# Kernel tuning notes

Hardware: AMD Instinct MI355X
Metric: run time of the kernel (lower is better)

The kernel has to match this reference:

```python
import jax, jax.numpy as jnp
import numpy as np

NUM_HEADS = 12
AGENT_NUM = 49

def setup_inputs() -> dict:
    key = jax.random.key(0)
    ks = jax.random.split(key, 5)
    B, N, C = 32, 1176, 768
    x = jax.random.normal(ks[0], (B, N, C), dtype=jnp.float32)
    qkv_w = jax.random.normal(ks[1], (3 * C, C), dtype=jnp.float32) * 0.02
    qkv_b = jax.random.normal(ks[2], (3 * C,), dtype=jnp.float32) * 0.02
    proj_w = jax.random.normal(ks[3], (C, C), dtype=jnp.float32) * 0.02
    proj_b = jax.random.normal(ks[4], (C,), dtype=jnp.float32) * 0.02
    return {"x": x, "qkv_w": qkv_w, "qkv_b": qkv_b, "proj_w": proj_w,
            "proj_b": proj_b, "t_h": 14, "t_w": 14, "s_h": 28, "s_w": 28}

def _softmax_clamped(a):
    # original: float32 clamp to finfo min/max, then softmax(dim=-1)
    fi = jnp.finfo(jnp.float32)
    a = jnp.clip(a.astype(jnp.float32), fi.min, fi.max)
    return jax.nn.softmax(a, axis=-1)

def reference(x, qkv_w, qkv_b, proj_w, proj_b, t_h, t_w, s_h, s_w):
    B, N, C = x.shape
    H = NUM_HEADS
    hd = C // H
    scale = hd ** -0.5
    n_mt = 2 * t_h * t_w
    n_s = s_h * s_w

    qkv = (x @ qkv_w.T + qkv_b).reshape(B, N, 3, H, hd).transpose(2, 0, 3, 1, 4)
    q, k, v = qkv[0], qkv[1], qkv[2]  # [B,H,N,hd]

    q_mt, q_s = q[:, :, :n_mt], q[:, :, n_mt:]
    k_mt = k[:, :, :n_mt]
    v_mt = v[:, :, :n_mt]

    # stage 1: template/memory self-attention
    attn = _softmax_clamped(jnp.einsum('bhqd,bhkd->bhqk', q_mt, k_mt) * scale)
    x_mt = jnp.einsum('bhqk,bhkd->bhqd', attn, v_mt).transpose(0, 2, 1, 3).reshape(B, n_mt, C)

    # agent tokens: pool q_s (replicates original layout-scrambling reshape)
    p = int(AGENT_NUM ** 0.5)  # 7
    agent = q_s.reshape(B, s_h, s_w, C).transpose(0, 3, 1, 2)  # [B,C,s_h,s_w]
    agent = agent.reshape(B, C, p, s_h // p, p, s_w // p).mean(axis=(3, 5))  # exact AdaptiveAvgPool2d(7,7)
    agent = agent.reshape(B, C, AGENT_NUM).transpose(0, 2, 1)  # [B,agent_num,C]
    agent = agent.reshape(B, AGENT_NUM, H, hd).transpose(0, 2, 1, 3)  # [B,H,agent_num,hd]

    # stage 2: agent attends to all keys
    agent_attn = _softmax_clamped(jnp.einsum('bhad,bhkd->bhak', agent * scale, k))
    agent_v = jnp.einsum('bhak,bhkd->bhad', agent_attn, v)  # [B,H,agent_num,hd]

    # stage 3: search queries attend to agent tokens
    q_attn = _softmax_clamped(jnp.einsum('bhqd,bhad->bhqa', q_s * scale, agent))
    x_s = jnp.einsum('bhqa,bhad->bhqd', q_attn, agent_v).transpose(0, 2, 1, 3).reshape(B, n_s, C)

    out = jnp.concatenate([x_mt, x_s], axis=1)
    out = out @ proj_w.T + proj_b
    return out
```

## Files before the change

### kernel.cpp

```cpp
#include <hip/hip_runtime.h>

typedef __attribute__((ext_vector_type(8))) short short8;
typedef __attribute__((ext_vector_type(4))) short short4v;
typedef __attribute__((ext_vector_type(4))) float f32x4;
typedef unsigned short u16;

#define B_    32
#define N_    1176
#define C_    768
#define H_    12
#define HD_   64
#define NMT_  392
#define AG_   49
#define NEGBIG_ (-1.0e4f)

__device__ __forceinline__ u16 f2bf(float f) {
  unsigned u = __float_as_uint(f);
  unsigned r = (u + 0x7fffu + ((u >> 16) & 1u)) >> 16;
  return (u16)r;
}
__device__ __forceinline__ float bf2f(u16 s) {
  return __uint_as_float(((unsigned)s) << 16);
}

__device__ __forceinline__ int xcd_swz(int g, int nwg) {
  const int q = nwg >> 3, r = nwg & 7;
  const int xcd = g & 7, off = g >> 3;
  return (xcd < r ? xcd * (q + 1) : r * (q + 1) + (xcd - r) * q) + off;
}

template <int LO>
__global__ __launch_bounds__(256) void splitf(const float* __restrict__ in,
                                              u16* __restrict__ hi,
                                              u16* __restrict__ lo, int n4) {
  int i = blockIdx.x * 256 + threadIdx.x;
  const int stride = gridDim.x * 256;
  for (; i < n4; i += stride) {
    const float4 v = ((const float4*)in)[i];
    const float f[4] = {v.x, v.y, v.z, v.w};
    short4v h, l;
#pragma unroll
    for (int e = 0; e < 4; ++e) {
      u16 hb = f2bf(f[e]);
      h[e] = (short)hb;
      if (LO) l[e] = (short)f2bf(f[e] - bf2f(hb));
    }
    ((short4v*)hi)[i] = h;
    if (LO) ((short4v*)lo)[i] = l;
  }
}

__global__ __launch_bounds__(256, 3) void gemm_qkv(
    const u16* __restrict__ A, const u16* __restrict__ Bw,
    const float* __restrict__ bias, u16* __restrict__ qb, u16* __restrict__ kb,
    u16* __restrict__ vb, int Mch) {
  __shared__ u16 SH[17408];
  u16* As = SH;
  u16* Bs = SH + 4096;
  const int tid = threadIdx.x;
  const int swz = xcd_swz(blockIdx.x, gridDim.x);
  const int brow = swz / 18, bcol = swz - brow * 18;
  const int m0 = brow * 128, c0 = bcol * 128;
  const int lane = tid & 63, w = tid >> 6;
  const int wr = w >> 1, wc = w & 1;
  const int fr = lane & 15, ko = lane >> 4;

  f32x4 acc[4][4];
#pragma unroll
  for (int m = 0; m < 4; ++m)
#pragma unroll
    for (int n = 0; n < 4; ++n) acc[m][n] = (f32x4)0.f;

  short8 ra[2], rb[2];
  auto LOADG = [&](int kt) {
#pragma unroll
    for (int i = 0; i < 2; ++i) {
      const int ch = tid + i * 256;
      const int row = ch >> 2, slot = ch & 3;
      const int ar = min(m0 + row, Mch - 1);
      ra[i] = *(const short8*)&A[(size_t)ar * 768 + kt * 32 + slot * 8];
      rb[i] = *(const short8*)&Bw[(size_t)(c0 + row) * 768 + kt * 32 + slot * 8];
    }
  };
  auto WRITE = [&]() {
#pragma unroll
    for (int i = 0; i < 2; ++i) {
      const int ch = tid + i * 256;
      const int row = ch >> 2, slot = ch & 3;
      const int off = (row >> 4) * 512 + slot * 128 + (row & 15) * 8;
      *(short8*)&As[off] = ra[i];
      *(short8*)&Bs[off] = rb[i];
    }
  };

  LOADG(0);
  for (int kt = 0; kt < 24; ++kt) {
    __syncthreads();
    WRITE();
    if (kt < 23) LOADG(kt + 1);
    __syncthreads();
    short8 af[4], bfr[4];
#pragma unroll
    for (int m = 0; m < 4; ++m) af[m] = *(const short8*)&As[(wr * 4 + m) * 512 + lane * 8];
#pragma unroll
    for (int n = 0; n < 4; ++n) bfr[n] = *(const short8*)&Bs[(wc * 4 + n) * 512 + lane * 8];
#pragma unroll
    for (int m = 0; m < 4; ++m)
#pragma unroll
      for (int n = 0; n < 4; ++n)
        acc[m][n] = __builtin_amdgcn_mfma_f32_16x16x32_bf16(af[m], bfr[n], acc[m][n], 0, 0, 0);
  }

  __syncthreads();
  const int t = c0 / 768;
  const int hbase = (c0 % 768) >> 6;
  if (t < 2) {
#pragma unroll
    for (int n = 0; n < 4; ++n) {
      const int col = wc * 64 + n * 16 + fr;
      const float bv = bias[c0 + col];
#pragma unroll
      for (int m = 0; m < 4; ++m)
#pragma unroll
        for (int r = 0; r < 4; ++r) {
          const int row = wr * 64 + m * 16 + ko * 4 + r;
          SH[row * 136 + col] = f2bf(acc[m][n][r] + bv);
        }
    }
    __syncthreads();
    u16* dst = (t == 0) ? qb : kb;
    for (int it = tid; it < 2048; it += 256) {
      const int rt = it >> 4, half = (it >> 3) & 1, p = it & 7;
      const int mg = m0 + rt;
      if (mg < Mch) {
        const int bl = mg / N_, nt = mg - bl * N_;
        const short8 vv = *(const short8*)&SH[rt * 136 + half * 64 + p * 8];
        *(short8*)&dst[(((size_t)bl * H_ + hbase + half) * N_ + nt) * 64 + p * 8] = vv;
      }
    }
  } else {
#pragma unroll
    for (int n = 0; n < 4; ++n) {
      const int col = wc * 64 + n * 16 + fr;
      const float bv = bias[c0 + col];
#pragma unroll
      for (int m = 0; m < 4; ++m)
#pragma unroll
        for (int r = 0; r < 4; ++r) {
          const int row = wr * 64 + m * 16 + ko * 4 + r;
          SH[col * 136 + row] = f2bf(acc[m][n][r] + bv);
        }
    }
    __syncthreads();
    for (int it = tid; it < 2048; it += 256) {
      const int ct = it >> 4, tc = it & 15;
      const int mg0 = m0 + tc * 8;
      if (mg0 < Mch) {
        const int bl = mg0 / N_, nt = mg0 - bl * N_;
        const int d = ct & 63, hh = hbase + (ct >> 6);
        const short8 vv = *(const short8*)&SH[ct * 136 + tc * 8];
        *(short8*)&vb[(((size_t)bl * H_ + hh) * 64 + d) * N_ + nt] = vv;
      }
    }
  }
}

__global__ __launch_bounds__(256, 2) void gemm_proj(
    const u16* __restrict__ Ahg, const u16* __restrict__ Alg,
    const u16* __restrict__ Bhg, const u16* __restrict__ Blg,
    const float* __restrict__ bias, float* __restrict__ out) {
  __shared__ u16 Ah[4096], Al[4096], Bh[4096], Bl[4096];
  const int tid = threadIdx.x;
  const int swz = xcd_swz(blockIdx.x, gridDim.x);
  const int brow = swz / 6, bcol = swz - brow * 6;
  const int m0 = brow * 128, c0 = bcol * 128;
  const int lane = tid & 63, w = tid >> 6;
  const int wr = w >> 1, wc = w & 1;
  const int fr = lane & 15, ko = lane >> 4;

  f32x4 acc[4][4];
#pragma unroll
  for (int m = 0; m < 4; ++m)
#pragma unroll
    for (int n = 0; n < 4; ++n) acc[m][n] = (f32x4)0.f;

  short8 rah[2], ral[2], rbh[2], rbl[2];
  auto LOADG = [&](int kt) {
#pragma unroll
    for (int i = 0; i < 2; ++i) {
      const int ch = tid + i * 256;
      const int row = ch >> 2, slot = ch & 3;
      const size_t aoff = (size_t)(m0 + row) * 768 + kt * 32 + slot * 8;
      const size_t boff = (size_t)(c0 + row) * 768 + kt * 32 + slot * 8;
      rah[i] = *(const short8*)&Ahg[aoff];
      ral[i] = *(const short8*)&Alg[aoff];
      rbh[i] = *(const short8*)&Bhg[boff];
      rbl[i] = *(const short8*)&Blg[boff];
    }
  };
  auto WRITE = [&]() {
#pragma unroll
    for (int i = 0; i < 2; ++i) {
      const int ch = tid + i * 256;
      const int row = ch >> 2, slot = ch & 3;
      const int off = (row >> 4) * 512 + slot * 128 + (row & 15) * 8;
      *(short8*)&Ah[off] = rah[i];
      *(short8*)&Al[off] = ral[i];
      *(short8*)&Bh[off] = rbh[i];
      *(short8*)&Bl[off] = rbl[i];
    }
  };

  LOADG(0);
  for (int kt = 0; kt < 24; ++kt) {
    __syncthreads();
    WRITE();
    if (kt < 23) LOADG(kt + 1);
    __syncthreads();
    short8 ah[4], al[4], bh[4], bl[4];
#pragma unroll
    for (int m = 0; m < 4; ++m) {
      ah[m] = *(const short8*)&Ah[(wr * 4 + m) * 512 + lane * 8];
      al[m] = *(const short8*)&Al[(wr * 4 + m) * 512 + lane * 8];
    }
#pragma unroll
    for (int n = 0; n < 4; ++n) {
      bh[n] = *(const short8*)&Bh[(wc * 4 + n) * 512 + lane * 8];
      bl[n] = *(const short8*)&Bl[(wc * 4 + n) * 512 + lane * 8];
    }
#pragma unroll
    for (int m = 0; m < 4; ++m)
#pragma unroll
      for (int n = 0; n < 4; ++n) {
        acc[m][n] = __builtin_amdgcn_mfma_f32_16x16x32_bf16(ah[m], bh[n], acc[m][n], 0, 0, 0);
        acc[m][n] = __builtin_amdgcn_mfma_f32_16x16x32_bf16(ah[m], bl[n], acc[m][n], 0, 0, 0);
        acc[m][n] = __builtin_amdgcn_mfma_f32_16x16x32_bf16(al[m], bh[n], acc[m][n], 0, 0, 0);
      }
  }
#pragma unroll
  for (int n = 0; n < 4; ++n) {
    const int col = c0 + wc * 64 + n * 16 + fr;
    const float bv = bias[col];
#pragma unroll
    for (int m = 0; m < 4; ++m) {
      const int mg = m0 + wr * 64 + m * 16 + ko * 4;
#pragma unroll
      for (int r = 0; r < 4; ++r) out[(size_t)(mg + r) * 768 + col] = acc[m][n][r] + bv;
    }
  }
}

__global__ __launch_bounds__(256) void agent_pool(const u16* __restrict__ q,
                                                  u16* __restrict__ agent) {
  const int wid = threadIdx.x >> 6;
  const int lane = threadIdx.x & 63;
  const int row = blockIdx.x * 4 + wid;
  const int rem = row % (H_ * 64);
  const int b = row / (H_ * 64);
  const int h2 = rem / 64;
  const int a = rem % 64;
  if (a >= AG_) {
    agent[((size_t)b * H_ + h2) * 4096 + a * 64 + lane] = 0;
    return;
  }
  const int ap = a / 7, aq = a % 7;
  float s = 0.f;
#pragma unroll
  for (int i = 0; i < 4; ++i)
#pragma unroll
    for (int j = 0; j < 4; ++j) {
      const int g = (ap * 4 + i) * 336 + (aq * 4 + j) * 12 + h2;
      const int h = g / 784, n = g % 784;
      s += bf2f(q[(((size_t)b * H_ + h) * N_ + NMT_ + n) * HD_ + lane]);
    }
  agent[((size_t)b * H_ + h2) * 4096 + a * 64 + lane] = f2bf(s * 0.0625f);
}

__global__ __launch_bounds__(256, 3) void flash_attn(
    const u16* __restrict__ Q, int q_bh_str, int q_base, int q_row_max, int q_valid,
    const u16* __restrict__ K, int k_bh_str, int k_row_max,
    const u16* __restrict__ Vt, int vt_bh_str, int vt_pitch, int vt_col_max,
    int n_keys, int nkt,
    u16* __restrict__ cch, u16* __restrict__ ccl, int b0,
    u16* __restrict__ avT, int mode) {
  __shared__ u16 Qs[4096], Ks[4096], Vts[4096], Ps[4096];
  __shared__ float Ss[64][65];
  __shared__ float mS[64], lS[64], aS[64];

  const int tid = threadIdx.x, bh = blockIdx.x;
  const int q0 = q_base + blockIdx.y * 56;
  const int lane = tid & 63, w = tid >> 6;
  const int fr = lane & 15, ko = lane >> 4;

  const u16* Qb = Q + (size_t)bh * q_bh_str;
  const u16* Kb = K + (size_t)bh * k_bh_str;
  const u16* Vb = Vt + (size_t)bh * vt_bh_str;

#pragma unroll
  for (int i = 0; i < 2; ++i) {
    const int ch = tid + i * 256;
    const int row = ch >> 3, c8 = (ch & 7) << 3;
    const int qr = min(q0 + row, q_row_max);
    const short8 v = *(const short8*)&Qb[(size_t)qr * 64 + c8];
    *(short8*)&Qs[(row * 64 + c8) ^ ((row & 7) << 3)] = v;
  }
  if (tid < 64) { mS[tid] = NEGBIG_; lS[tid] = 0.f; aS[tid] = 0.f; }

  f32x4 oacc[4];
#pragma unroll
  for (int d = 0; d < 4; ++d) oacc[d] = (f32x4)0.f;

  for (int kt = 0; kt < nkt; ++kt) {
#pragma unroll
    for (int i = 0; i < 2; ++i) {
      const int ch = tid + i * 256;
      const int row = ch >> 3, c8 = (ch & 7) << 3;
      const int kr = min(kt * 64 + row, k_row_max);
      const short8 v = *(const short8*)&Kb[(size_t)kr * 64 + c8];
      *(short8*)&Ks[(row * 64 + c8) ^ ((row & 7) << 3)] = v;
    }
#pragma unroll
    for (int i = 0; i < 2; ++i) {
      const int ch = tid + i * 256;
      const int row = ch >> 3, c8 = (ch & 7) << 3;
      const int col8 = kt * 64 + c8;
      const u16* src = &Vb[(size_t)row * vt_pitch];
      short8 v;
      if (col8 + 8 <= vt_col_max) {
        v = *(const short8*)&src[col8];
      } else {
#pragma unroll
        for (int e = 0; e < 8; ++e) v[e] = (short)src[min(col8 + e, vt_col_max - 1)];
      }
      *(short8*)&Vts[(row * 64 + c8) ^ ((row & 7) << 3)] = v;
    }
    __syncthreads();

    short8 aq[2];
#pragma unroll
    for (int s = 0; s < 2; ++s)
      aq[s] = *(const short8*)&Qs[((w * 16 + fr) * 64 + s * 32 + ko * 8) ^ ((fr & 7) << 3)];
#pragma unroll
    for (int j = 0; j < 4; ++j) {
      f32x4 sa = (f32x4)0.f;
#pragma unroll
      for (int s = 0; s < 2; ++s) {
        const short8 bk = *(const short8*)&Ks[((j * 16 + fr) * 64 + s * 32 + ko * 8) ^ ((fr & 7) << 3)];
        sa = __builtin_amdgcn_mfma_f32_16x16x32_bf16(aq[s], bk, sa, 0, 0, 0);
      }
      const int colg = kt * 64 + j * 16 + fr;
      const bool maskc = (colg >= n_keys);
#pragma unroll
      for (int r = 0; r < 4; ++r) {
        const int srow = w * 16 + ko * 4 + r;
        Ss[srow][j * 16 + fr] = maskc ? NEGBIG_ : sa[r] * 0.125f;
      }
    }
    __syncthreads();

    {
      const int r = tid >> 2, jj = tid & 3;
      float sv[16];
      float mx = NEGBIG_;
#pragma unroll
      for (int c = 0; c < 16; ++c) {
        sv[c] = Ss[r][jj * 16 + c];
        mx = fmaxf(mx, sv[c]);
      }
      mx = fmaxf(mx, __shfl_xor(mx, 1));
      mx = fmaxf(mx, __shfl_xor(mx, 2));
      const float mold = mS[r];
      const float mnew = fmaxf(mold, mx);
      float sum = 0.f;
#pragma unroll
      for (int c = 0; c < 16; ++c) {
        const bool mk = (kt * 64 + jj * 16 + c) >= n_keys;
        const float p = mk ? 0.f : __expf(sv[c] - mnew);
        sum += p;
        Ps[(r * 64 + jj * 16 + c) ^ ((r & 7) << 3)] = f2bf(p);
      }
      sum += __shfl_xor(sum, 1);
      sum += __shfl_xor(sum, 2);
      if (jj == 0) {
        const float alpha = __expf(mold - mnew);
        aS[r] = alpha;
        lS[r] = lS[r] * alpha + sum;
        mS[r] = mnew;
      }
    }
    __syncthreads();

    float al[4];
#pragma unroll
    for (int r = 0; r < 4; ++r) al[r] = aS[w * 16 + ko * 4 + r];
    short8 ap[2];
#pragma unroll
    for (int s = 0; s < 2; ++s)
      ap[s] = *(const short8*)&Ps[((w * 16 + fr) * 64 + s * 32 + ko * 8) ^ ((fr & 7) << 3)];
#pragma unroll
    for (int dj = 0; dj < 4; ++dj) {
      f32x4 o = oacc[dj];
#pragma unroll
      for (int r = 0; r < 4; ++r) o[r] *= al[r];
#pragma unroll
      for (int s = 0; s < 2; ++s) {
        const short8 bv = *(const short8*)&Vts[((dj * 16 + fr) * 64 + s * 32 + ko * 8) ^ ((fr & 7) << 3)];
        o = __builtin_amdgcn_mfma_f32_16x16x32_bf16(ap[s], bv, o, 0, 0, 0);
      }
      oacc[dj] = o;
    }
    __syncthreads();
  }

  float linv[4];
#pragma unroll
  for (int r = 0; r < 4; ++r) linv[r] = 1.f / fmaxf(lS[w * 16 + ko * 4 + r], 1e-30f);

  if (mode == 0) {
    const int b = bh / H_, h = bh % H_;
#pragma unroll
    for (int dj = 0; dj < 4; ++dj)
#pragma unroll
      for (int r = 0; r < 4; ++r) {
        const int rowl = w * 16 + ko * 4 + r;
        if (rowl < q_valid) {
          const size_t m = (size_t)(b0 + b) * N_ + q0 + rowl;
          const float val = oacc[dj][r] * linv[r];
          const u16 hb = f2bf(val);
          const u16 lb = f2bf(val - bf2f(hb));
          const size_t idx = m * 768 + h * 64 + dj * 16 + fr;
          cch[idx] = hb;
          ccl[idx] = lb;
        }
      }
  } else {
#pragma unroll
    for (int dj = 0; dj < 4; ++dj)
#pragma unroll
      for (int r = 0; r < 4; ++r) {
        const int a = w * 16 + ko * 4 + r;
        avT[(size_t)bh * 4096 + (dj * 16 + fr) * 64 + a] = f2bf(oacc[dj][r] * linv[r]);
      }
  }
}

extern "C" void kernel_launch(void* const* d_in, const int* in_sizes, int n_in,
                              void* d_out, int out_size, void* d_ws,
                              size_t ws_size, hipStream_t stream) {
  const float* x = (const float*)d_in[0];
  const float* qkv_w = (const float*)d_in[1];
  const float* qkv_b = (const float*)d_in[2];
  const float* proj_w = (const float*)d_in[3];
  const float* proj_b = (const float*)d_in[4];
  float* out = (float*)d_out;
  u16* ws = (u16*)d_ws;

  const size_t XBF = 28901376ull;
  const size_t QW = 2304ull * 768;
  const size_t PW = 768ull * 768;
  const size_t QKV1 = (size_t)H_ * N_ * HD_;
  const size_t AG1 = (size_t)H_ * 64 * 64;

  size_t o = 0;
  u16* xbf = ws + o; o += XBF;
  u16* qwh = ws + o; o += QW;
  u16* pwh = ws + o; o += PW;
  u16* pwl = ws + o; o += PW;
  u16* cch = ws + o; o += XBF;
  u16* ccl = ws + o; o += XBF;
  const size_t fixed_sh = o;
  const size_t per_sh = 3 * QKV1 + 2 * AG1;

  int cb = 1;
  const int cands[6] = {32, 16, 8, 4, 2, 1};
  for (int i = 0; i < 6; ++i)
    if ((fixed_sh + (size_t)cands[i] * per_sh) * 2 <= ws_size) { cb = cands[i]; break; }

  u16* qb = ws + o; o += cb * QKV1;
  u16* kb = ws + o; o += cb * QKV1;
  u16* vb = ws + o; o += cb * QKV1;
  u16* agent = ws + o; o += cb * AG1;
  u16* avT = ws + o; o += cb * AG1;

  splitf<0><<<2048, 256, 0, stream>>>(x, xbf, nullptr, (int)(XBF / 4));
  splitf<0><<<1024, 256, 0, stream>>>(qkv_w, qwh, nullptr, (int)(QW / 4));
  splitf<1><<<512, 256, 0, stream>>>(proj_w, pwh, pwl, (int)(PW / 4));

  const int nch = B_ / cb;
  for (int chn = 0; chn < nch; ++chn) {
    const int b0 = chn * cb;
    const int Mch = cb * N_;
    const int nrow = (Mch + 127) / 128;
    gemm_qkv<<<dim3(nrow * 18), 256, 0, stream>>>(
        xbf + (size_t)b0 * N_ * 768, qwh, qkv_b, qb, kb, vb, Mch);
    agent_pool<<<dim3(cb * 192), 256, 0, stream>>>(qb, agent);
    flash_attn<<<dim3(cb * H_, 1), 256, 0, stream>>>(
        agent, 4096, 0, 48, AG_, kb, N_ * HD_, N_ - 1,
        vb, N_ * HD_, N_, N_, N_, 19, nullptr, nullptr, b0, avT, 1);
    flash_attn<<<dim3(cb * H_, 7), 256, 0, stream>>>(
        qb, N_ * HD_, 0, N_ - 1, 56, kb, N_ * HD_, N_ - 1,
        vb, N_ * HD_, N_, N_, NMT_, 7, cch, ccl, b0, nullptr, 0);
    flash_attn<<<dim3(cb * H_, 14), 256, 0, stream>>>(
        qb, N_ * HD_, NMT_, N_ - 1, 56, agent, 4096, 63,
        avT, 4096, 64, 64, AG_, 1, cch, ccl, b0, nullptr, 0);
  }
  gemm_proj<<<dim3(294 * 6), 256, 0, stream>>>(cch, ccl, pwh, pwl, proj_b, out);
}
```

Measured before the change: 552.9 us.

## Fuse x fp32-to-bf16 conversion into QKV GEMM loads and drop epilogue barrier

The QKV GEMM now reads x directly in fp32 and rounds it to bf16 while staging it into shared memory. This removes the separate conversion pass over x and its bf16 workspace copy, which saves a full write and re-read of a roughly 58 MB buffer. The global load mapping now writes each wave's MFMA fragment layout directly, in both GEMMs. The epilogue stages output per wave with padded rows, so the block-wide barrier is gone. In exchange the GEMM fetches twice the A bytes per tile and does the rounding inside its main loop.

```diff
diff --git a/kernel.cpp b/kernel.cpp
--- a/kernel.cpp
+++ b/kernel.cpp
@@ -51,7 +51,7 @@
 }
 
 __global__ __launch_bounds__(256, 3) void gemm_qkv(
-    const u16* __restrict__ A, const u16* __restrict__ Bw,
+    const float* __restrict__ A, const u16* __restrict__ Bw,
     const float* __restrict__ bias, u16* __restrict__ qb, u16* __restrict__ kb,
     u16* __restrict__ vb, int Mch) {
   __shared__ u16 SH[17408];
@@ -71,25 +71,30 @@
 #pragma unroll
     for (int n = 0; n < 4; ++n) acc[m][n] = (f32x4)0.f;
 
-  short8 ra[2], rb[2];
+  float4 raf[2][2];
+  short8 rb[2];
   auto LOADG = [&](int kt) {
 #pragma unroll
     for (int i = 0; i < 2; ++i) {
-      const int ch = tid + i * 256;
-      const int row = ch >> 2, slot = ch & 3;
-      const int ar = min(m0 + row, Mch - 1);
-      ra[i] = *(const short8*)&A[(size_t)ar * 768 + kt * 32 + slot * 8];
-      rb[i] = *(const short8*)&Bw[(size_t)(c0 + row) * 768 + kt * 32 + slot * 8];
+      const int g = w * 2 + i;
+      const int ar = min(m0 + g * 16 + fr, Mch - 1);
+      const float* pa = &A[(size_t)ar * 768 + kt * 32 + ko * 8];
+      raf[i][0] = *(const float4*)pa;
+      raf[i][1] = *(const float4*)(pa + 4);
+      rb[i] = *(const short8*)&Bw[(size_t)(c0 + g * 16 + fr) * 768 + kt * 32 + ko * 8];
     }
   };
   auto WRITE = [&]() {
 #pragma unroll
     for (int i = 0; i < 2; ++i) {
-      const int ch = tid + i * 256;
-      const int row = ch >> 2, slot = ch & 3;
-      const int off = (row >> 4) * 512 + slot * 128 + (row & 15) * 8;
-      *(short8*)&As[off] = ra[i];
-      *(short8*)&Bs[off] = rb[i];
+      const int g = w * 2 + i;
+      const float fa[8] = {raf[i][0].x, raf[i][0].y, raf[i][0].z, raf[i][0].w,
+                           raf[i][1].x, raf[i][1].y, raf[i][1].z, raf[i][1].w};
+      short8 ha;
+#pragma unroll
+      for (int e = 0; e < 8; ++e) ha[e] = (short)f2bf(fa[e]);
+      *(short8*)&As[g * 512 + lane * 8] = ha;
+      *(short8*)&Bs[g * 512 + lane * 8] = rb[i];
     }
   };
 
@@ -112,54 +117,51 @@
   }
 
   __syncthreads();
-  const int t = c0 / 768;
-  const int hbase = (c0 % 768) >> 6;
+  u16* SHW = SH + w * 4352;
+  const int colbase = c0 + wc * 64;
+  const int t = colbase / 768;
+  const int hh = (colbase % 768) >> 6;
   if (t < 2) {
 #pragma unroll
     for (int n = 0; n < 4; ++n) {
-      const int col = wc * 64 + n * 16 + fr;
-      const float bv = bias[c0 + col];
+      const float bv = bias[colbase + n * 16 + fr];
 #pragma unroll
       for (int m = 0; m < 4; ++m)
 #pragma unroll
-        for (int r = 0; r < 4; ++r) {
-          const int row = wr * 64 + m * 16 + ko * 4 + r;
-          SH[row * 136 + col] = f2bf(acc[m][n][r] + bv);
-        }
-    }
-    __syncthreads();
+        for (int r = 0; r < 4; ++r)
+          SHW[(m * 16 + ko * 4 + r) * 68 + n * 16 + fr] = f2bf(acc[m][n][r] + bv);
+    }
     u16* dst = (t == 0) ? qb : kb;
-    for (int it = tid; it < 2048; it += 256) {
-      const int rt = it >> 4, half = (it >> 3) & 1, p = it & 7;
-      const int mg = m0 + rt;
+#pragma unroll
+    for (int it = 0; it < 8; ++it) {
+      const int idx = lane + it * 64;
+      const int rowl = idx >> 3, pc = idx & 7;
+      const int mg = m0 + wr * 64 + rowl;
       if (mg < Mch) {
         const int bl = mg / N_, nt = mg - bl * N_;
-        const short8 vv = *(const short8*)&SH[rt * 136 + half * 64 + p * 8];
-        *(short8*)&dst[(((size_t)bl * H_ + hbase + half) * N_ + nt) * 64 + p * 8] = vv;
+        *(short8*)&dst[(((size_t)bl * H_ + hh) * N_ + nt) * 64 + pc * 8] =
+            *(const short8*)&SHW[rowl * 68 + pc * 8];
       }
     }
   } else {
 #pragma unroll
     for (int n = 0; n < 4; ++n) {
-      const int col = wc * 64 + n * 16 + fr;
-      const float bv = bias[c0 + col];
+      const float bv = bias[colbase + n * 16 + fr];
 #pragma unroll
       for (int m = 0; m < 4; ++m)
 #pragma unroll
-        for (int r = 0; r < 4; ++r) {
-          const int row = wr * 64 + m * 16 + ko * 4 + r;
-          SH[col * 136 + row] = f2bf(acc[m][n][r] + bv);
-        }
-    }
-    __syncthreads();
-    for (int it = tid; it < 2048; it += 256) {
-      const int ct = it >> 4, tc = it & 15;
-      const int mg0 = m0 + tc * 8;
+        for (int r = 0; r < 4; ++r)
+          SHW[(n * 16 + fr) * 68 + m * 16 + ko * 4 + r] = f2bf(acc[m][n][r] + bv);
+    }
+#pragma unroll
+    for (int it = 0; it < 8; ++it) {
+      const int idx = lane + it * 64;
+      const int d = idx >> 3, pc = idx & 7;
+      const int mg0 = m0 + wr * 64 + pc * 8;
       if (mg0 < Mch) {
         const int bl = mg0 / N_, nt = mg0 - bl * N_;
-        const int d = ct & 63, hh = hbase + (ct >> 6);
-        const short8 vv = *(const short8*)&SH[ct * 136 + tc * 8];
-        *(short8*)&vb[(((size_t)bl * H_ + hh) * 64 + d) * N_ + nt] = vv;
+        *(short8*)&vb[(((size_t)bl * H_ + hh) * 64 + d) * N_ + nt] =
+            *(const short8*)&SHW[d * 68 + pc * 8];
       }
     }
   }
@@ -188,10 +190,9 @@
   auto LOADG = [&](int kt) {
 #pragma unroll
     for (int i = 0; i < 2; ++i) {
-      const int ch = tid + i * 256;
-      const int row = ch >> 2, slot = ch & 3;
-      const size_t aoff = (size_t)(m0 + row) * 768 + kt * 32 + slot * 8;
-      const size_t boff = (size_t)(c0 + row) * 768 + kt * 32 + slot * 8;
+      const int g = w * 2 + i;
+      const size_t aoff = (size_t)(m0 + g * 16 + fr) * 768 + kt * 32 + ko * 8;
+      const size_t boff = (size_t)(c0 + g * 16 + fr) * 768 + kt * 32 + ko * 8;
       rah[i] = *(const short8*)&Ahg[aoff];
       ral[i] = *(const short8*)&Alg[aoff];
       rbh[i] = *(const short8*)&Bhg[boff];
@@ -201,13 +202,11 @@
   auto WRITE = [&]() {
 #pragma unroll
     for (int i = 0; i < 2; ++i) {
-      const int ch = tid + i * 256;
-      const int row = ch >> 2, slot = ch & 3;
-      const int off = (row >> 4) * 512 + slot * 128 + (row & 15) * 8;
-      *(short8*)&Ah[off] = rah[i];
-      *(short8*)&Al[off] = ral[i];
-      *(short8*)&Bh[off] = rbh[i];
-      *(short8*)&Bl[off] = rbl[i];
+      const int g = w * 2 + i;
+      *(short8*)&Ah[g * 512 + lane * 8] = rah[i];
+      *(short8*)&Al[g * 512 + lane * 8] = ral[i];
+      *(short8*)&Bh[g * 512 + lane * 8] = rbh[i];
+      *(short8*)&Bl[g * 512 + lane * 8] = rbl[i];
     }
   };
 
@@ -462,7 +461,6 @@
   const size_t AG1 = (size_t)H_ * 64 * 64;
 
   size_t o = 0;
-  u16* xbf = ws + o; o += XBF;
   u16* qwh = ws + o; o += QW;
   u16* pwh = ws + o; o += PW;
   u16* pwl = ws + o; o += PW;
@@ -482,7 +480,6 @@
   u16* agent = ws + o; o += cb * AG1;
   u16* avT = ws + o; o += cb * AG1;
 
-  splitf<0><<<2048, 256, 0, stream>>>(x, xbf, nullptr, (int)(XBF / 4));
   splitf<0><<<1024, 256, 0, stream>>>(qkv_w, qwh, nullptr, (int)(QW / 4));
   splitf<1><<<512, 256, 0, stream>>>(proj_w, pwh, pwl, (int)(PW / 4));
 
@@ -492,7 +489,7 @@
     const int Mch = cb * N_;
     const int nrow = (Mch + 127) / 128;
     gemm_qkv<<<dim3(nrow * 18), 256, 0, stream>>>(
-        xbf + (size_t)b0 * N_ * 768, qwh, qkv_b, qb, kb, vb, Mch);
+        x + (size_t)b0 * N_ * 768, qwh, qkv_b, qb, kb, vb, Mch);
     agent_pool<<<dim3(cb * 192), 256, 0, stream>>>(qb, agent);
     flash_attn<<<dim3(cb * H_, 1), 256, 0, stream>>>(
         agent, 4096, 0, 48, AG_, kb, N_ * HD_, N_ - 1,
```

Result: slower. 751.6 us (+35.9%).
